# Kernel tuning notes

Measured on AMD Instinct MI355X. Metric: run time of the kernel, lower is better.

Reference implementation:

```python
import jax, jax.numpy as jnp
import numpy as np

S, B, L = 512, 256, 128  # seq_length, batch_size, label_nums
PAD_ID, START_ID = 0, 1


def setup_inputs() -> dict:
    key = jax.random.key(0)
    k1, k2, k3, k4 = jax.random.split(key, 4)
    emit_scores = jax.random.normal(k1, (S, B, L), dtype=jnp.float32)
    labels = jax.random.randint(k2, (B, S), 0, L, dtype=jnp.int32)
    # contiguous prefix masks: lengths in [1, S]
    lengths = jax.random.randint(k3, (B,), 1, S + 1, dtype=jnp.int32)
    masks = jnp.arange(S, dtype=jnp.int32)[None, :] < lengths[:, None]  # (B, S) bool
    T = jax.random.normal(k4, (L, L), dtype=jnp.float32) * 0.1  # transition params
    return {"emit_scores": emit_scores, "labels": labels, "masks": masks, "T": T}


def reference(emit_scores, labels, masks, T):
    seq_len, batch, label_nums = emit_scores.shape

    # ---- gold path score (calc_sentences_scores) ----
    lengths = masks.astype(jnp.int32).sum(axis=1)                       # (B,)
    ends_index = jnp.take_along_axis(labels, (lengths - 1)[:, None], axis=1)[:, 0]
    ends_scores = T[ends_index, PAD_ID].sum()

    labels_ext = jnp.concatenate(
        [jnp.full((batch, 1), START_ID, dtype=labels.dtype), labels], axis=1)  # (B, S+1)
    prev = labels_ext[:, :-1]                                           # (B, S)
    nxt = labels                                                        # (B, S)
    emit_bt = jnp.transpose(emit_scores, (1, 0, 2))                     # (B, S, L)
    emit_sel = jnp.take_along_axis(emit_bt, nxt[:, :, None], axis=2)[:, :, 0]  # (B, S)
    trans_sel = T[prev, nxt]                                            # (B, S)
    gold = jnp.where(masks, emit_sel + trans_sel, 0.0).sum() + ends_scores

    # ---- partition function (crf_encode): log-sum-exp scan over time ----
    fs0 = emit_scores[0] + T[START_ID][None, :]                         # (B, L)

    def step(fs, inp):
        e_t, m_t = inp                                                  # (B, L), (B,)
        # scores[b, i, j] = fs[b, i] + T[i, j] + e_t[b, j]
        scores = fs[:, :, None] + T[None, :, :] + e_t[:, None, :]
        cur = jax.nn.logsumexp(scores, axis=1)                          # (B, L)
        fs = jnp.where(m_t[:, None], cur, fs)
        return fs, None

    fs, _ = jax.lax.scan(step, fs0, (emit_scores[1:], masks.T[1:]))
    encode = jax.nn.logsumexp(fs + T[:, PAD_ID][None, :], axis=1).sum()

    return encode - gold
```

## Files before the change

kernel.cpp:

```cpp
#include <hip/hip_runtime.h>
#include <hip/hip_fp8.h>

#define S_LEN 512
#define BATCH 256
#define L 128
#define PAD_ID 0
#define START_ID 1

typedef int    i32x8 __attribute__((ext_vector_type(8)));
typedef int    i32x4 __attribute__((ext_vector_type(4)));
typedef float  f32x4 __attribute__((ext_vector_type(4)));
typedef unsigned int   u32x4 __attribute__((ext_vector_type(4)));
typedef unsigned short u16x2 __attribute__((ext_vector_type(2)));

__device__ __forceinline__ unsigned int umax2(unsigned int a, unsigned int b) {
    u16x2 x = __builtin_bit_cast(u16x2, a), y = __builtin_bit_cast(u16x2, b);
#if defined(__has_builtin) && __has_builtin(__builtin_elementwise_max)
    return __builtin_bit_cast(unsigned int, __builtin_elementwise_max(x, y));
#else
    u16x2 r; r.x = x.x > y.x ? x.x : y.x; r.y = x.y > y.y ? x.y : y.y;
    return __builtin_bit_cast(unsigned int, r);
#endif
}
__device__ __forceinline__ float frcp(float x) {
#if defined(__has_builtin) && __has_builtin(__builtin_amdgcn_rcpf)
    return __builtin_amdgcn_rcpf(x);
#else
    return 1.0f / x;
#endif
}
__device__ __forceinline__ float sane(float x, float lo, float hi) {
    return fminf(fmaxf(x, lo), hi);
}
__device__ __forceinline__ int pk2_fp8(float a, float b) {
#if defined(__has_builtin) && __has_builtin(__builtin_amdgcn_cvt_pk_fp8_f32)
    return __builtin_amdgcn_cvt_pk_fp8_f32(a, b, 0, false);
#else
    __hip_fp8_e4m3 A(a), B(b);
    return (int)A.__x | ((int)B.__x << 8);
#endif
}
__device__ __forceinline__ unsigned int bmax8(u32x4 a, u32x4 b) {
    const unsigned int M = 0x00FF00FFu;
    unsigned int l0 = umax2(a.x & M, a.y & M), l1 = umax2(a.z & M, a.w & M);
    unsigned int l2 = umax2(b.x & M, b.y & M), l3 = umax2(b.z & M, b.w & M);
    unsigned int h0 = umax2((a.x >> 8) & M, (a.y >> 8) & M);
    unsigned int h1 = umax2((a.z >> 8) & M, (a.w >> 8) & M);
    unsigned int h2 = umax2((b.x >> 8) & M, (b.y >> 8) & M);
    unsigned int h3 = umax2((b.z >> 8) & M, (b.w >> 8) & M);
    unsigned int v = umax2(umax2(umax2(l0, l1), umax2(l2, l3)),
                           umax2(umax2(h0, h1), umax2(h2, h3)));
    u16x2 t = __builtin_bit_cast(u16x2, v);
    return (unsigned int)(t.x > t.y ? t.x : t.y);
}
__device__ __forceinline__ float fp8dec(unsigned int bb) {
    bb &= 0x7Fu;
    int e = (int)(bb >> 3), mt = (int)(bb & 7u);
    float v = e ? __builtin_ldexpf((float)(8 + mt), e - 10)
                : __builtin_ldexpf((float)mt, -9);
    return sane(v, 1e-9f, 448.f);
}

#define WS_QF 0
#define WS_QB 32768
#define WS_SF 65536
#define WS_SB 66560
#define WS_N  67584

__device__ __forceinline__ int compute_len(const void* masks, int b, int lane) {
    const unsigned int* mw0 = (const unsigned int*)masks;
    int pred = 0;
    #pragma unroll
    for (int k = 0; k < 32; ++k) {
        unsigned int w0 = mw0[lane + 64 * k];
        pred |= (w0 > 1u && w0 != 0x3f800000u);
    }
    const bool isbyte = (__ballot(pred) != 0ull);
    int cnt = 0;
    if (isbyte) {
        const unsigned int* mw = mw0 + b * (S_LEN / 4);
        #pragma unroll
        for (int k = 0; k < 2; ++k) {
            unsigned int w0 = mw[lane + 64 * k];
            cnt += ((w0 & 0xffu) != 0) + ((w0 & 0xff00u) != 0) +
                   ((w0 & 0xff0000u) != 0) + ((w0 & 0xff000000u) != 0);
        }
    } else {
        const unsigned int* mw = mw0 + b * S_LEN;
        #pragma unroll
        for (int k = 0; k < 8; ++k) cnt += (mw[lane + 64 * k] != 0u);
    }
    #pragma unroll
    for (int off = 32; off; off >>= 1) cnt += __shfl_xor(cnt, off, 64);
    return cnt;
}

__global__ __launch_bounds__(64, 1) void k_scan(
        const float* __restrict__ emit, const int* __restrict__ labels,
        const void* __restrict__ masks, const float* __restrict__ T,
        unsigned char* __restrict__ ws, float* __restrict__ out) {
    const int bid  = blockIdx.x;
    const int lane = threadIdx.x;

    if (bid >= 2 * BATCH) {
        const int b = bid - 2 * BATCH;
        const int len = compute_len(masks, b, lane);
        float gsum = 0.f;
        for (int tt = lane; tt < len; tt += 64) {
            int nxt = labels[b * S_LEN + tt];
            int prv = tt ? labels[b * S_LEN + tt - 1] : START_ID;
            gsum += emit[((size_t)tt * BATCH + b) * L + nxt] + T[prv * L + nxt];
            if (tt == len - 1) gsum += T[nxt * L + PAD_ID];
        }
        #pragma unroll
        for (int off = 32; off; off >>= 1) gsum += __shfl_xor(gsum, off, 64);
        if (lane == 0) atomicAdd(out, -gsum);
        return;
    }

    const int b   = bid & (BATCH - 1);
    const int dir = bid >> 8;
    const int g = lane >> 4, m = lane & 15;

    const int len = compute_len(masks, b, lane);
    const int n  = len - 1;
    const int kf = n / 2;
    const int nB = n - kf - 1;
    const int steps = dir ? (nB > 0 ? nB : 0) : kf;
    if (dir == 1 && n < 1) return;

    const int tm = m >> 1;
    const int j1 = 16 * tm + 4 * g + 2 * (m & 1);
    const int s1 = 8 * (j1 & 15) + tm;

    __shared__ __align__(16) unsigned char st[128];

    i32x8 Af[8];
    #pragma unroll
    for (int t = 0; t < 8; ++t) {
        #pragma unroll
        for (int d = 0; d < 8; ++d) {
            float v[4];
            #pragma unroll
            for (int y = 0; y < 4; ++y) {
                int sl = 4 * d + y;
                int k  = 16 * (sl & 7) + 4 * g + (sl >> 3);
                int idx = dir ? ((16 * t + m) * L + k) : (k * L + 16 * t + m);
                v[y] = __expf(T[idx]);
            }
            int p01 = pk2_fp8(v[0], v[1]), p23 = pk2_fp8(v[2], v[3]);
            Af[t][d] = (p01 & 0xffff) | (p23 << 16);
        }
    }

    float f1, f2;
    if (dir == 0) {
        f1 = emit[(size_t)b * L + j1]     + T[START_ID * L + j1];
        f2 = emit[(size_t)b * L + j1 + 1] + T[START_ID * L + j1 + 1];
    } else {
        const float* er = emit + ((size_t)n * BATCH + b) * L;
        f1 = er[j1]     + T[j1 * L + PAD_ID];
        f2 = er[j1 + 1] + T[(j1 + 1) * L + PAD_ID];
    }
    float S;
    {
        float mx = fmaxf(f1, f2);
        #pragma unroll
        for (int off = 32; off; off >>= 1) mx = fmaxf(mx, __shfl_xor(mx, off, 64));
        S = mx;
    }
    {
        float p0 = sane(__expf(f1 - S), 1e-9f, 400.f);
        float p1 = sane(__expf(f2 - S), 1e-9f, 400.f);
        int pk = pk2_fp8(p0, p1);
        st[s1]     = (unsigned char)(pk & 0xff);
        st[s1 + 8] = (unsigned char)((pk >> 8) & 0xff);
    }
    asm volatile("s_waitcnt lgkmcnt(0)" ::: "memory");
    i32x4 alo = *(const i32x4*)&st[32 * g];
    i32x4 ahi = *(const i32x4*)&st[32 * g + 16];

    const f32x4 z = {0.f, 0.f, 0.f, 0.f};
    const int base1 = b * L + j1;

    if (steps > 0) {
        auto ldrow = [&](int idx) -> float2 {
            int ii  = idx < steps - 1 ? idx : steps - 1;
            int row = dir ? (n - 1 - ii) : (1 + ii);
            return *(const float2*)(emit + (size_t)row * (BATCH * L) + base1);
        };
        float2 eb0 = ldrow(0), eb1 = ldrow(1), eb2 = ldrow(2), eb3 = ldrow(3);
        int i = 0;

#define MFS(AT) __builtin_amdgcn_mfma_scale_f32_16x16x128_f8f6f4((AT), Aq, z, 0, 0, 0, 127, 0, 127)
#define STEP(EB)                                                               \
        {                                                                      \
            i32x8 Aq;                                                          \
            Aq[0] = alo[0]; Aq[1] = alo[1]; Aq[2] = alo[2]; Aq[3] = alo[3];    \
            Aq[4] = ahi[0]; Aq[5] = ahi[1]; Aq[6] = ahi[2]; Aq[7] = ahi[3];    \
            f32x4 d0 = MFS(Af[0]), d1 = MFS(Af[1]), d2 = MFS(Af[2]),           \
                  d3 = MFS(Af[3]), d4 = MFS(Af[4]), d5 = MFS(Af[5]),           \
                  d6 = MFS(Af[6]), d7 = MFS(Af[7]);                            \
            unsigned int qm = bmax8(__builtin_bit_cast(u32x4, alo),            \
                                    __builtin_bit_cast(u32x4, ahi));           \
            {                                                                  \
                unsigned int q2 = (unsigned int)__shfl_xor((int)qm, 16, 64);   \
                qm = qm > q2 ? qm : q2;                                        \
                q2 = (unsigned int)__shfl_xor((int)qm, 32, 64);                \
                qm = qm > q2 ? qm : q2;                                        \
            }                                                                  \
            float msc = fp8dec(qm);                                            \
            float kk  = frcp(msc);                                             \
            float xe0 = __expf(EB.x) * kk, xe1 = __expf(EB.y) * kk;            \
            const bool sr = (m & 1) != 0, sB = (m & 2) != 0,                   \
                       sC = (m & 4) != 0, sD = (m & 8) != 0;                   \
            float a0 = sr ? d0[2] : d0[0], b0 = sr ? d0[3] : d0[1];            \
            float a1 = sr ? d1[2] : d1[0], b1 = sr ? d1[3] : d1[1];            \
            float a2 = sr ? d2[2] : d2[0], b2 = sr ? d2[3] : d2[1];            \
            float a3 = sr ? d3[2] : d3[0], b3 = sr ? d3[3] : d3[1];            \
            float a4 = sr ? d4[2] : d4[0], b4 = sr ? d4[3] : d4[1];            \
            float a5 = sr ? d5[2] : d5[0], b5 = sr ? d5[3] : d5[1];            \
            float a6 = sr ? d6[2] : d6[0], b6 = sr ? d6[3] : d6[1];            \
            float a7 = sr ? d7[2] : d7[0], b7 = sr ? d7[3] : d7[1];            \
            float aA = sB ? a1 : a0, aB2 = sB ? a3 : a2;                       \
            float aC = sB ? a5 : a4, aD2 = sB ? a7 : a6;                       \
            float bA = sB ? b1 : b0, bB2 = sB ? b3 : b2;                       \
            float bC = sB ? b5 : b4, bD2 = sB ? b7 : b6;                       \
            float aE = sC ? aB2 : aA, aF = sC ? aD2 : aC;                      \
            float bE = sC ? bB2 : bA, bF = sC ? bD2 : bC;                      \
            float c0 = sD ? aF : aE, c1 = sD ? bF : bE;                        \
            float p0 = sane(c0 * xe0, 1e-9f, 400.f);                           \
            float p1 = sane(c1 * xe1, 1e-9f, 400.f);                           \
            int pk = pk2_fp8(p0, p1);                                          \
            st[s1]     = (unsigned char)(pk & 0xff);                           \
            st[s1 + 8] = (unsigned char)((pk >> 8) & 0xff);                    \
            asm volatile("s_waitcnt lgkmcnt(0)" ::: "memory");                 \
            alo = *(const i32x4*)&st[32 * g];                                  \
            ahi = *(const i32x4*)&st[32 * g + 16];                             \
            S += __logf(msc);                                                  \
        }

        for (;;) {
            STEP(eb0); eb0 = ldrow(i + 4); if (++i == steps) break;
            STEP(eb1); eb1 = ldrow(i + 4); if (++i == steps) break;
            STEP(eb2); eb2 = ldrow(i + 4); if (++i == steps) break;
            STEP(eb3); eb3 = ldrow(i + 4); if (++i == steps) break;
        }
#undef STEP
#undef MFS
    }

    if (m == 0) {
        i32x4* sp = (i32x4*)(ws + (dir ? WS_QB : WS_QF) + b * L + 32 * g);
        sp[0] = alo; sp[1] = ahi;
    }
    if (lane == 0) {
        ((float*)(ws + (dir ? WS_SB : WS_SF)))[b] = S;
        if (dir == 0) ((int*)(ws + WS_N))[b] = n;
    }
}

__global__ __launch_bounds__(64, 1) void k_join(
        const float* __restrict__ T, const unsigned char* __restrict__ ws,
        float* __restrict__ out) {
    const int b = blockIdx.x;
    const int lane = threadIdx.x;
    __shared__ float qsh[L], ush[L];

    const int n = ((const int*)(ws + WS_N))[b];
    #pragma unroll
    for (int k = 0; k < 2; ++k) {
        int s = lane + 64 * k;
        int j = 16 * (s & 7) + (s >> 3);
        qsh[j] = fp8dec(ws[WS_QF + b * L + s]);
        ush[j] = fp8dec(ws[WS_QB + b * L + s]);
    }
    __syncthreads();

    float ev = 0.f;
    if (n >= 1) {
        #pragma unroll
        for (int k = 0; k < 2; ++k) {
            int j = lane + 64 * k;
            float v = 0.f;
            for (int i = 0; i < L; ++i)
                v = fmaf(qsh[i], __expf(T[i * L + j]), v);
            ev += v * ush[j];
        }
    } else {
        #pragma unroll
        for (int k = 0; k < 2; ++k) {
            int j = lane + 64 * k;
            ev += qsh[j] * __expf(T[j * L + PAD_ID]);
        }
    }
    #pragma unroll
    for (int off = 32; off; off >>= 1) ev += __shfl_xor(ev, off, 64);

    if (lane == 0) {
        float Sf = ((const float*)(ws + WS_SF))[b];
        float Sb = (n >= 1) ? ((const float*)(ws + WS_SB))[b] : 0.f;
        float enc = Sf + Sb + __logf(fmaxf(ev, 1e-35f));
        atomicAdd(out, sane(enc, -1e30f, 1e30f));
    }
}

extern "C" void kernel_launch(void* const* d_in, const int* in_sizes, int n_in,
                              void* d_out, int out_size, void* d_ws, size_t ws_size,
                              hipStream_t stream) {
    const float* emit   = (const float*)d_in[0];
    const int*   labels = (const int*)d_in[1];
    const void*  masks  = d_in[2];
    const float* T      = (const float*)d_in[3];
    float* out = (float*)d_out;
    unsigned char* ws = (unsigned char*)d_ws;

    hipMemsetAsync(d_out, 0, sizeof(float), stream);
    k_scan<<<dim3(3 * BATCH), dim3(64), 0, stream>>>(emit, labels, masks, T, ws, out);
    k_join<<<dim3(BATCH),     dim3(64), 0, stream>>>(T, ws, out);
}
```

Measured before the change: 247.3 us.

## Keep CRF forward state in registers across MFMA steps instead of LDS round-trip

Each lane now computes all 32 state values it needs for the next MFMA operand straight from the accumulator outputs, so the per-step LDS store/wait/reload and the select-tree shuffling are gone. The reciprocal/log rescale is replaced by an exact power-of-two scale built from the fp8 exponent, summed as an integer and converted once at the end. The join kernel's inner dot product gets four independent accumulators. In exchange each lane does 16x more exp and pack work per step and holds three 32-float emission prefetch buffers, which raises register pressure.

```diff
diff --git a/kernel.cpp b/kernel.cpp
--- a/kernel.cpp
+++ b/kernel.cpp
@@ -22,22 +22,16 @@
     return __builtin_bit_cast(unsigned int, r);
 #endif
 }
-__device__ __forceinline__ float frcp(float x) {
-#if defined(__has_builtin) && __has_builtin(__builtin_amdgcn_rcpf)
-    return __builtin_amdgcn_rcpf(x);
-#else
-    return 1.0f / x;
-#endif
-}
 __device__ __forceinline__ float sane(float x, float lo, float hi) {
     return fminf(fmaxf(x, lo), hi);
 }
-__device__ __forceinline__ int pk2_fp8(float a, float b) {
+__device__ __forceinline__ int pk4(float a, float b, float c, float d) {
 #if defined(__has_builtin) && __has_builtin(__builtin_amdgcn_cvt_pk_fp8_f32)
-    return __builtin_amdgcn_cvt_pk_fp8_f32(a, b, 0, false);
+    int lo = __builtin_amdgcn_cvt_pk_fp8_f32(a, b, 0, false);
+    return __builtin_amdgcn_cvt_pk_fp8_f32(c, d, lo, true);
 #else
-    __hip_fp8_e4m3 A(a), B(b);
-    return (int)A.__x | ((int)B.__x << 8);
+    __hip_fp8_e4m3 A(a), B(b), C(c), D(d);
+    return (int)A.__x | ((int)B.__x << 8) | ((int)C.__x << 16) | ((int)D.__x << 24);
 #endif
 }
 __device__ __forceinline__ unsigned int bmax8(u32x4 a, u32x4 b) {
@@ -60,6 +54,16 @@
                 : __builtin_ldexpf((float)mt, -9);
     return sane(v, 1e-9f, 448.f);
 }
+__device__ __forceinline__ f32x4 vexp4(f32x4 x) {
+    f32x4 r;
+    r.x = __expf(x.x); r.y = __expf(x.y); r.z = __expf(x.z); r.w = __expf(x.w);
+    return r;
+}
+__device__ __forceinline__ f32x4 vmin4(f32x4 a, float c) {
+    f32x4 r;
+    r.x = fminf(a.x, c); r.y = fminf(a.y, c); r.z = fminf(a.z, c); r.w = fminf(a.w, c);
+    return r;
+}
 
 #define WS_QF 0
 #define WS_QB 32768
@@ -129,12 +133,6 @@
     const int steps = dir ? (nB > 0 ? nB : 0) : kf;
     if (dir == 1 && n < 1) return;
 
-    const int tm = m >> 1;
-    const int j1 = 16 * tm + 4 * g + 2 * (m & 1);
-    const int s1 = 8 * (j1 & 15) + tm;
-
-    __shared__ __align__(16) unsigned char st[128];
-
     i32x8 Af[8];
     #pragma unroll
     for (int t = 0; t < 8; ++t) {
@@ -148,103 +146,107 @@
                 int idx = dir ? ((16 * t + m) * L + k) : (k * L + 16 * t + m);
                 v[y] = __expf(T[idx]);
             }
-            int p01 = pk2_fp8(v[0], v[1]), p23 = pk2_fp8(v[2], v[3]);
-            Af[t][d] = (p01 & 0xffff) | (p23 << 16);
-        }
-    }
-
-    float f1, f2;
-    if (dir == 0) {
-        f1 = emit[(size_t)b * L + j1]     + T[START_ID * L + j1];
-        f2 = emit[(size_t)b * L + j1 + 1] + T[START_ID * L + j1 + 1];
-    } else {
-        const float* er = emit + ((size_t)n * BATCH + b) * L;
-        f1 = er[j1]     + T[j1 * L + PAD_ID];
-        f2 = er[j1 + 1] + T[(j1 + 1) * L + PAD_ID];
-    }
-    float S;
+            Af[t][d] = pk4(v[0], v[1], v[2], v[3]);
+        }
+    }
+
+    float S_base;
+    i32x8 Aq;
     {
-        float mx = fmaxf(f1, f2);
-        #pragma unroll
-        for (int off = 32; off; off >>= 1) mx = fmaxf(mx, __shfl_xor(mx, off, 64));
-        S = mx;
-    }
-    {
-        float p0 = sane(__expf(f1 - S), 1e-9f, 400.f);
-        float p1 = sane(__expf(f2 - S), 1e-9f, 400.f);
-        int pk = pk2_fp8(p0, p1);
-        st[s1]     = (unsigned char)(pk & 0xff);
-        st[s1 + 8] = (unsigned char)((pk >> 8) & 0xff);
-    }
-    asm volatile("s_waitcnt lgkmcnt(0)" ::: "memory");
-    i32x4 alo = *(const i32x4*)&st[32 * g];
-    i32x4 ahi = *(const i32x4*)&st[32 * g + 16];
-
+        f32x4 fv[8];
+        const float* e0 = emit + (dir ? ((size_t)n * BATCH + b) * L : (size_t)b * L);
+        #pragma unroll
+        for (int t = 0; t < 8; ++t) {
+            int k0 = 16 * t + 4 * g;
+            f32x4 ev4 = *(const f32x4*)(e0 + k0);
+            f32x4 tv;
+            if (dir == 0) {
+                tv = *(const f32x4*)(T + START_ID * L + k0);
+            } else {
+                tv.x = T[(k0 + 0) * L + PAD_ID];
+                tv.y = T[(k0 + 1) * L + PAD_ID];
+                tv.z = T[(k0 + 2) * L + PAD_ID];
+                tv.w = T[(k0 + 3) * L + PAD_ID];
+            }
+            fv[t] = ev4 + tv;
+        }
+        float mx = -1e30f;
+        #pragma unroll
+        for (int t = 0; t < 8; ++t)
+            mx = fmaxf(mx, fmaxf(fmaxf(fv[t].x, fv[t].y), fmaxf(fv[t].z, fv[t].w)));
+        mx = fmaxf(mx, __shfl_xor(mx, 16, 64));
+        mx = fmaxf(mx, __shfl_xor(mx, 32, 64));
+        S_base = mx;
+        f32x4 pv[8];
+        #pragma unroll
+        for (int t = 0; t < 8; ++t) pv[t] = vexp4(fv[t] - S_base);
+        Aq[0] = pk4(pv[0].x, pv[1].x, pv[2].x, pv[3].x);
+        Aq[1] = pk4(pv[4].x, pv[5].x, pv[6].x, pv[7].x);
+        Aq[2] = pk4(pv[0].y, pv[1].y, pv[2].y, pv[3].y);
+        Aq[3] = pk4(pv[4].y, pv[5].y, pv[6].y, pv[7].y);
+        Aq[4] = pk4(pv[0].z, pv[1].z, pv[2].z, pv[3].z);
+        Aq[5] = pk4(pv[4].z, pv[5].z, pv[6].z, pv[7].z);
+        Aq[6] = pk4(pv[0].w, pv[1].w, pv[2].w, pv[3].w);
+        Aq[7] = pk4(pv[4].w, pv[5].w, pv[6].w, pv[7].w);
+    }
+
+    int Se = 0;
     const f32x4 z = {0.f, 0.f, 0.f, 0.f};
-    const int base1 = b * L + j1;
 
     if (steps > 0) {
-        auto ldrow = [&](int idx) -> float2 {
-            int ii  = idx < steps - 1 ? idx : steps - 1;
+        auto ldrow8 = [&](int idx, f32x4* dst) {
+            int ii  = idx < steps ? idx : steps - 1;
             int row = dir ? (n - 1 - ii) : (1 + ii);
-            return *(const float2*)(emit + (size_t)row * (BATCH * L) + base1);
+            const float* ep = emit + ((size_t)row * BATCH + b) * L + 4 * g;
+            #pragma unroll
+            for (int t = 0; t < 8; ++t) dst[t] = *(const f32x4*)(ep + 16 * t);
         };
-        float2 eb0 = ldrow(0), eb1 = ldrow(1), eb2 = ldrow(2), eb3 = ldrow(3);
+        f32x4 ea[8], eb[8], ec[8];
+        ldrow8(0, ea); ldrow8(1, eb); ldrow8(2, ec);
         int i = 0;
 
 #define MFS(AT) __builtin_amdgcn_mfma_scale_f32_16x16x128_f8f6f4((AT), Aq, z, 0, 0, 0, 127, 0, 127)
-#define STEP(EB)                                                               \
-        {                                                                      \
-            i32x8 Aq;                                                          \
-            Aq[0] = alo[0]; Aq[1] = alo[1]; Aq[2] = alo[2]; Aq[3] = alo[3];    \
-            Aq[4] = ahi[0]; Aq[5] = ahi[1]; Aq[6] = ahi[2]; Aq[7] = ahi[3];    \
-            f32x4 d0 = MFS(Af[0]), d1 = MFS(Af[1]), d2 = MFS(Af[2]),           \
-                  d3 = MFS(Af[3]), d4 = MFS(Af[4]), d5 = MFS(Af[5]),           \
-                  d6 = MFS(Af[6]), d7 = MFS(Af[7]);                            \
-            unsigned int qm = bmax8(__builtin_bit_cast(u32x4, alo),            \
-                                    __builtin_bit_cast(u32x4, ahi));           \
-            {                                                                  \
-                unsigned int q2 = (unsigned int)__shfl_xor((int)qm, 16, 64);   \
-                qm = qm > q2 ? qm : q2;                                        \
-                q2 = (unsigned int)__shfl_xor((int)qm, 32, 64);                \
-                qm = qm > q2 ? qm : q2;                                        \
-            }                                                                  \
-            float msc = fp8dec(qm);                                            \
-            float kk  = frcp(msc);                                             \
-            float xe0 = __expf(EB.x) * kk, xe1 = __expf(EB.y) * kk;            \
-            const bool sr = (m & 1) != 0, sB = (m & 2) != 0,                   \
-                       sC = (m & 4) != 0, sD = (m & 8) != 0;                   \
-            float a0 = sr ? d0[2] : d0[0], b0 = sr ? d0[3] : d0[1];            \
-            float a1 = sr ? d1[2] : d1[0], b1 = sr ? d1[3] : d1[1];            \
-            float a2 = sr ? d2[2] : d2[0], b2 = sr ? d2[3] : d2[1];            \
-            float a3 = sr ? d3[2] : d3[0], b3 = sr ? d3[3] : d3[1];            \
-            float a4 = sr ? d4[2] : d4[0], b4 = sr ? d4[3] : d4[1];            \
-            float a5 = sr ? d5[2] : d5[0], b5 = sr ? d5[3] : d5[1];            \
-            float a6 = sr ? d6[2] : d6[0], b6 = sr ? d6[3] : d6[1];            \
-            float a7 = sr ? d7[2] : d7[0], b7 = sr ? d7[3] : d7[1];            \
-            float aA = sB ? a1 : a0, aB2 = sB ? a3 : a2;                       \
-            float aC = sB ? a5 : a4, aD2 = sB ? a7 : a6;                       \
-            float bA = sB ? b1 : b0, bB2 = sB ? b3 : b2;                       \
-            float bC = sB ? b5 : b4, bD2 = sB ? b7 : b6;                       \
-            float aE = sC ? aB2 : aA, aF = sC ? aD2 : aC;                      \
-            float bE = sC ? bB2 : bA, bF = sC ? bD2 : bC;                      \
-            float c0 = sD ? aF : aE, c1 = sD ? bF : bE;                        \
-            float p0 = sane(c0 * xe0, 1e-9f, 400.f);                           \
-            float p1 = sane(c1 * xe1, 1e-9f, 400.f);                           \
-            int pk = pk2_fp8(p0, p1);                                          \
-            st[s1]     = (unsigned char)(pk & 0xff);                           \
-            st[s1 + 8] = (unsigned char)((pk >> 8) & 0xff);                    \
-            asm volatile("s_waitcnt lgkmcnt(0)" ::: "memory");                 \
-            alo = *(const i32x4*)&st[32 * g];                                  \
-            ahi = *(const i32x4*)&st[32 * g + 16];                             \
-            S += __logf(msc);                                                  \
+#define STEP(EB)                                                                   \
+        {                                                                          \
+            f32x4 d0 = MFS(Af[0]), d1 = MFS(Af[1]), d2 = MFS(Af[2]), d3 = MFS(Af[3]); \
+            f32x4 d4 = MFS(Af[4]), d5 = MFS(Af[5]), d6 = MFS(Af[6]), d7 = MFS(Af[7]); \
+            f32x4 x0 = vexp4(EB[0]), x1 = vexp4(EB[1]), x2 = vexp4(EB[2]),         \
+                  x3 = vexp4(EB[3]), x4 = vexp4(EB[4]), x5 = vexp4(EB[5]),         \
+                  x6 = vexp4(EB[6]), x7 = vexp4(EB[7]);                            \
+            u32x4 qlo = {(unsigned)Aq[0], (unsigned)Aq[1],                         \
+                         (unsigned)Aq[2], (unsigned)Aq[3]};                        \
+            u32x4 qhi = {(unsigned)Aq[4], (unsigned)Aq[5],                         \
+                         (unsigned)Aq[6], (unsigned)Aq[7]};                        \
+            unsigned int qm = bmax8(qlo, qhi);                                     \
+            {                                                                      \
+                unsigned int q2 = (unsigned int)__shfl_xor((int)qm, 16, 64);       \
+                qm = qm > q2 ? qm : q2;                                            \
+                q2 = (unsigned int)__shfl_xor((int)qm, 32, 64);                    \
+                qm = qm > q2 ? qm : q2;                                            \
+            }                                                                      \
+            int e7 = (int)(qm >> 3) - 7;                                           \
+            Se += e7;                                                              \
+            float kk = __builtin_bit_cast(float, (unsigned int)(127 - e7) << 23);  \
+            x0 *= kk; x1 *= kk; x2 *= kk; x3 *= kk;                                \
+            x4 *= kk; x5 *= kk; x6 *= kk; x7 *= kk;                                \
+            f32x4 p0 = vmin4(d0 * x0, 448.f), p1 = vmin4(d1 * x1, 448.f);          \
+            f32x4 p2 = vmin4(d2 * x2, 448.f), p3 = vmin4(d3 * x3, 448.f);          \
+            f32x4 p4 = vmin4(d4 * x4, 448.f), p5 = vmin4(d5 * x5, 448.f);          \
+            f32x4 p6 = vmin4(d6 * x6, 448.f), p7 = vmin4(d7 * x7, 448.f);          \
+            Aq[0] = pk4(p0.x, p1.x, p2.x, p3.x);                                   \
+            Aq[1] = pk4(p4.x, p5.x, p6.x, p7.x);                                   \
+            Aq[2] = pk4(p0.y, p1.y, p2.y, p3.y);                                   \
+            Aq[3] = pk4(p4.y, p5.y, p6.y, p7.y);                                   \
+            Aq[4] = pk4(p0.z, p1.z, p2.z, p3.z);                                   \
+            Aq[5] = pk4(p4.z, p5.z, p6.z, p7.z);                                   \
+            Aq[6] = pk4(p0.w, p1.w, p2.w, p3.w);                                   \
+            Aq[7] = pk4(p4.w, p5.w, p6.w, p7.w);                                   \
         }
 
         for (;;) {
-            STEP(eb0); eb0 = ldrow(i + 4); if (++i == steps) break;
-            STEP(eb1); eb1 = ldrow(i + 4); if (++i == steps) break;
-            STEP(eb2); eb2 = ldrow(i + 4); if (++i == steps) break;
-            STEP(eb3); eb3 = ldrow(i + 4); if (++i == steps) break;
+            STEP(ea); if (++i == steps) break; ldrow8(i + 2, ea);
+            STEP(eb); if (++i == steps) break; ldrow8(i + 2, eb);
+            STEP(ec); if (++i == steps) break; ldrow8(i + 2, ec);
         }
 #undef STEP
 #undef MFS
@@ -252,10 +254,11 @@
 
     if (m == 0) {
         i32x4* sp = (i32x4*)(ws + (dir ? WS_QB : WS_QF) + b * L + 32 * g);
-        sp[0] = alo; sp[1] = ahi;
+        sp[0] = (i32x4){Aq[0], Aq[1], Aq[2], Aq[3]};
+        sp[1] = (i32x4){Aq[4], Aq[5], Aq[6], Aq[7]};
     }
     if (lane == 0) {
-        ((float*)(ws + (dir ? WS_SB : WS_SF)))[b] = S;
+        ((float*)(ws + (dir ? WS_SB : WS_SF)))[b] = S_base + 0.69314718f * (float)Se;
         if (dir == 0) ((int*)(ws + WS_N))[b] = n;
     }
 }
@@ -282,10 +285,15 @@
         #pragma unroll
         for (int k = 0; k < 2; ++k) {
             int j = lane + 64 * k;
-            float v = 0.f;
-            for (int i = 0; i < L; ++i)
-                v = fmaf(qsh[i], __expf(T[i * L + j]), v);
-            ev += v * ush[j];
+            float v0 = 0.f, v1 = 0.f, v2 = 0.f, v3 = 0.f;
+            #pragma unroll 8
+            for (int i = 0; i < L; i += 4) {
+                v0 = fmaf(qsh[i + 0], __expf(T[(i + 0) * L + j]), v0);
+                v1 = fmaf(qsh[i + 1], __expf(T[(i + 1) * L + j]), v1);
+                v2 = fmaf(qsh[i + 2], __expf(T[(i + 2) * L + j]), v2);
+                v3 = fmaf(qsh[i + 3], __expf(T[(i + 3) * L + j]), v3);
+            }
+            ev += ((v0 + v1) + (v2 + v3)) * ush[j];
         }
     } else {
         #pragma unroll
```

Result: slower. 304.7 us (+23.2%).
